# Kernel optimization log

Hardware: AMD Instinct MI355X
Metric: run time of the kernel (lower is better)

The kernel has to match this reference:

```python
import jax, jax.numpy as jnp
import numpy as np

ALPHA = 1.702  # sigmoid slope in clamped-GLU
LIMIT = 7.0    # clamp limit on gate/up

B, S, H, D, E, K = 2, 2048, 1024, 1024, 8, 2


def setup_inputs() -> dict:
    key = jax.random.key(0)
    ks = jax.random.split(key, 7)
    hidden_states = jax.random.normal(ks[0], (B, S, H), jnp.float32)
    router_indices = jax.random.randint(ks[1], (B * S, K), 0, E)
    routing_weights = jax.random.uniform(ks[2], (B * S, E), dtype=jnp.float32)
    gate_up_proj = jax.random.normal(ks[3], (E, H, 2 * D), jnp.float32) * 0.02
    gate_up_bias = jax.random.normal(ks[4], (E, 2 * D), jnp.float32) * 0.02
    down_proj = jax.random.normal(ks[5], (E, D, H), jnp.float32) * 0.02
    down_bias = jax.random.normal(ks[6], (E, H), jnp.float32) * 0.02
    return dict(hidden_states=hidden_states, router_indices=router_indices,
                routing_weights=routing_weights, gate_up_proj=gate_up_proj,
                gate_up_bias=gate_up_bias, down_proj=down_proj, down_bias=down_bias)


def reference(hidden_states, router_indices, routing_weights,
              gate_up_proj, gate_up_bias, down_proj, down_bias):
    batch = hidden_states.shape[0]
    hs = hidden_states.shape[-1]
    flat = hidden_states.reshape(-1, hs)  # [T, H]
    n_exp = routing_weights.shape[1]
    # index_add with possibly duplicated (token, expert) assignments == count multiplier
    counts = (router_indices[:, :, None] == jnp.arange(n_exp)[None, None, :]).sum(1)  # [T, E]
    w = routing_weights * counts.astype(flat.dtype)  # [T, E] effective combine weight

    def step(out, xs):
        wgu, bgu, wd, bd, we = xs  # wgu:[H,2D] bgu:[2D] wd:[D,H] bd:[H] we:[T]
        gu = flat @ wgu + bgu                      # [T, 2D]
        gate = jnp.minimum(gu[:, ::2], LIMIT)      # interleaved gate channels
        up = jnp.clip(gu[:, 1::2], -LIMIT, LIMIT)  # interleaved up channels
        mid = (up + 1.0) * gate * jax.nn.sigmoid(gate * ALPHA)
        y = mid @ wd + bd                          # [T, H]
        return out + y * we[:, None], None

    out0 = jnp.zeros_like(flat)
    out, _ = jax.lax.scan(step, out0, (gate_up_proj, gate_up_bias, down_proj, down_bias, w.T))
    return out.reshape(batch, -1, hs)
```

## Files before the change

### kernel.cpp

```cpp
#include <hip/hip_runtime.h>
#include <hip/hip_bf16.h>

#define AS1 __attribute__((address_space(1)))
#define AS3 __attribute__((address_space(3)))

typedef __bf16 bf16_8 __attribute__((ext_vector_type(8)));
typedef float f32x4 __attribute__((ext_vector_type(4)));

constexpr int Tn = 4096;
constexpr int Hn = 1024;
constexpr int Dn = 1024;
constexpr int En = 8;
constexpr int Pmax = 9216;
constexpr int MaxTiles = 72;
constexpr float kAlpha = 1.702f;
constexpr float kLimit = 7.0f;

__device__ __forceinline__ unsigned short f2bf(float x) {
  unsigned u = __builtin_bit_cast(unsigned, x);
  u = u + 0x7FFFu + ((u >> 16) & 1u);
  return (unsigned short)(u >> 16);
}
__device__ __forceinline__ unsigned pack2(float a, float b) {
  return (unsigned)f2bf(a) | ((unsigned)f2bf(b) << 16);
}
__device__ __forceinline__ float bflo(unsigned v) { return __builtin_bit_cast(float, v << 16); }
__device__ __forceinline__ float bfhi(unsigned v) { return __builtin_bit_cast(float, v & 0xFFFF0000u); }

__device__ __forceinline__ void gload_lds16(const void* gp, void* lp) {
  __builtin_amdgcn_global_load_lds(
      (const AS1 unsigned int*)(unsigned long long)gp,
      (AS3 unsigned int*)(unsigned int)(unsigned long long)lp,
      16, 0, 0);
}

constexpr int NB_CVT = 4096, NB_TGU = 4096, NB_TDN = 4096;
constexpr int NG1 = MaxTiles * (Dn / 64);

__global__ void k_prepass(const float* __restrict__ hs, const int* __restrict__ ridx,
                          const float* __restrict__ gup,
                          unsigned short* __restrict__ xb,
                          unsigned short* __restrict__ wg, unsigned short* __restrict__ wu,
                          int* __restrict__ tix, int* __restrict__ pos,
                          int* __restrict__ tileE, int* __restrict__ tileP0,
                          int* __restrict__ ntiles) {
  __shared__ __align__(16) char smem[2 * 32 * 65 * 4 + 64];
  const int tid = threadIdx.x;
  int b = blockIdx.x;

  if (b == 0) {
    int (*lh)[8] = (int(*)[8])smem;
    int* eoff = (int*)(smem + 8192);
#pragma unroll
    for (int e = 0; e < 8; e++) lh[tid][e] = 0;
    int myE[32];
#pragma unroll
    for (int s = 0; s < 32; s++) {
      int e = ridx[tid * 32 + s];
      myE[s] = e;
      lh[tid][e]++;
    }
    __syncthreads();
    if (tid < 8) {
      int tot = 0;
#pragma unroll 1
      for (int t = 0; t < 256; t++) { int v = lh[t][tid]; lh[t][tid] = tot; tot += v; }
      eoff[tid] = tot;
    }
    __syncthreads();
    if (tid == 0) {
      int off = 0, nt = 0;
#pragma unroll 1
      for (int e = 0; e < 8; e++) {
        int cnt = eoff[e];
        eoff[e] = off;
        int nt128 = (cnt + 127) >> 7;
        for (int k = 0; k < nt128; k++) { tileE[nt] = e; tileP0[nt] = off + k * 128; nt++; }
        off += nt128 * 128;
      }
      *ntiles = nt;
    }
    __syncthreads();
    for (int p = tid; p < Pmax; p += 256) tix[p] = 0;
    __syncthreads();
#pragma unroll
    for (int s = 0; s < 32; s++) {
      int slot = tid * 32 + s;
      int e = myE[s];
      int p = eoff[e] + (lh[tid][e]++);
      pos[slot] = p;
      tix[p] = slot >> 1;
    }
    return;
  }
  b -= 1;

  if (b < NB_CVT) {
    int i = b * 256 + tid;
    float4 v = reinterpret_cast<const float4*>(hs)[i];
    ushort4 o;
    o.x = f2bf(v.x); o.y = f2bf(v.y); o.z = f2bf(v.z); o.w = f2bf(v.w);
    reinterpret_cast<ushort4*>(xb)[i] = o;
    return;
  }
  b -= NB_CVT;

  {
    float (*lg)[65] = (float(*)[65])smem;
    float (*lu)[65] = (float(*)[65])(smem + 32 * 65 * 4);
    const int d0 = (b & 31) * 32, h0 = ((b >> 5) & 15) * 64, e = b >> 9;
    {
      const int hrow = tid >> 2, q = tid & 3;
      const float* src = gup + ((size_t)e * Hn + h0 + hrow) * (2 * Dn) + d0 * 2 + q * 16;
#pragma unroll
      for (int j = 0; j < 4; j++) {
        float4 v = *reinterpret_cast<const float4*>(src + j * 4);
        int dp = q * 8 + j * 2;
        lg[dp][hrow] = v.x; lu[dp][hrow] = v.y;
        lg[dp + 1][hrow] = v.z; lu[dp + 1][hrow] = v.w;
      }
    }
    __syncthreads();
    {
      const int d = tid >> 3, hc = (tid & 7) * 8;
      uint4 og, ou;
      og.x = pack2(lg[d][hc + 0], lg[d][hc + 1]); ou.x = pack2(lu[d][hc + 0], lu[d][hc + 1]);
      og.y = pack2(lg[d][hc + 2], lg[d][hc + 3]); ou.y = pack2(lu[d][hc + 2], lu[d][hc + 3]);
      og.z = pack2(lg[d][hc + 4], lg[d][hc + 5]); ou.z = pack2(lu[d][hc + 4], lu[d][hc + 5]);
      og.w = pack2(lg[d][hc + 6], lg[d][hc + 7]); ou.w = pack2(lu[d][hc + 6], lu[d][hc + 7]);
      *reinterpret_cast<uint4*>(wg + ((size_t)e * Dn + d0 + d) * Hn + h0 + hc) = og;
      *reinterpret_cast<uint4*>(wu + ((size_t)e * Dn + d0 + d) * Hn + h0 + hc) = ou;
    }
  }
}

__launch_bounds__(256, 2)
__global__ void k_main1(const unsigned short* __restrict__ xb,
                        const unsigned short* __restrict__ wg,
                        const unsigned short* __restrict__ wu,
                        const float* __restrict__ gub,
                        const int* __restrict__ tix,
                        const int* __restrict__ tileE,
                        const int* __restrict__ tileP0,
                        const int* __restrict__ ntiles,
                        unsigned short* __restrict__ midc,
                        const float* __restrict__ dwn,
                        unsigned short* __restrict__ wdt) {
  constexpr int BM = 128, BN = 64, BK = 64;
  __shared__ __align__(16) char smem[(BM + 2 * BN) * BK * 2];
  const int tid = threadIdx.x;

  if ((int)blockIdx.x >= NG1) {
    int b = blockIdx.x - NG1;
    float (*lt)[65] = (float(*)[65])smem;
    const int h0 = (b & 31) * 32, d0 = ((b >> 5) & 15) * 64, e = b >> 9;
    {
      const int drow = tid >> 2, q = tid & 3;
      const float* src = dwn + ((size_t)e * Dn + d0 + drow) * Hn + h0 + q * 8;
#pragma unroll
      for (int j = 0; j < 2; j++) {
        float4 v = *reinterpret_cast<const float4*>(src + j * 4);
        int hr = q * 8 + j * 4;
        lt[hr][drow] = v.x; lt[hr + 1][drow] = v.y; lt[hr + 2][drow] = v.z; lt[hr + 3][drow] = v.w;
      }
    }
    __syncthreads();
    {
      const int h = tid >> 3, dc = (tid & 7) * 8;
      uint4 o;
      o.x = pack2(lt[h][dc + 0], lt[h][dc + 1]);
      o.y = pack2(lt[h][dc + 2], lt[h][dc + 3]);
      o.z = pack2(lt[h][dc + 4], lt[h][dc + 5]);
      o.w = pack2(lt[h][dc + 6], lt[h][dc + 7]);
      *reinterpret_cast<uint4*>(wdt + ((size_t)e * Hn + h0 + h) * Dn + d0 + dc) = o;
    }
    return;
  }

  unsigned short* Xs = (unsigned short*)smem;
  unsigned short* Gs = (unsigned short*)(smem + BM * BK * 2);
  unsigned short* Us = (unsigned short*)(smem + (BM + BN) * BK * 2);
  const int orig = blockIdx.x;
  const int wgid = (orig & 7) * (NG1 >> 3) + (orig >> 3);
  const int bx = wgid % MaxTiles;
  const int by = wgid / MaxTiles;
  if (bx >= *ntiles) return;
  const int e = tileE[bx];
  const int p0 = tileP0[bx];
  const int n0 = by * BN;
  const int wv = tid >> 6, lane = tid & 63;
  const int wr = wv >> 1, wc = wv & 1;
  const int r8 = lane >> 3, c8 = lane & 7;

  int tokc[4];
#pragma unroll
  for (int c = 0; c < 4; c++) tokc[c] = tix[p0 + (c * 4 + wv) * 8 + r8];

  const unsigned short* Gp = wg + ((size_t)e * Dn + n0) * Hn;
  const unsigned short* Up = wu + ((size_t)e * Dn + n0) * Hn;

  f32x4 ag[4][2], au[4][2];
#pragma unroll
  for (int i = 0; i < 4; i++)
#pragma unroll
    for (int j = 0; j < 2; j++) { ag[i][j] = f32x4{0.f,0.f,0.f,0.f}; au[i][j] = f32x4{0.f,0.f,0.f,0.f}; }

  for (int k0 = 0; k0 < Hn; k0 += BK) {
#pragma unroll
    for (int c = 0; c < 4; c++) {
      int ch = c * 4 + wv;
      gload_lds16(xb + (size_t)tokc[c] * Hn + k0 + c8 * 8, (void*)(Xs + ch * 512));
    }
#pragma unroll
    for (int c = 0; c < 2; c++) {
      int ch = c * 4 + wv;
      gload_lds16(Gp + (size_t)(ch * 8 + r8) * Hn + k0 + c8 * 8, (void*)(Gs + ch * 512));
      gload_lds16(Up + (size_t)(ch * 8 + r8) * Hn + k0 + c8 * 8, (void*)(Us + ch * 512));
    }
    asm volatile("s_waitcnt vmcnt(0)" ::: "memory");
    __syncthreads();
    const int fr = lane & 15, kg = lane >> 4;
#pragma unroll
    for (int kk = 0; kk < 2; kk++) {
      bf16_8 a[4], bg[2], bu[2];
#pragma unroll
      for (int i = 0; i < 4; i++)
        a[i] = *reinterpret_cast<const bf16_8*>(Xs + (wr * 64 + i * 16 + fr) * BK + kk * 32 + kg * 8);
#pragma unroll
      for (int j = 0; j < 2; j++) {
        bg[j] = *reinterpret_cast<const bf16_8*>(Gs + (wc * 32 + j * 16 + fr) * BK + kk * 32 + kg * 8);
        bu[j] = *reinterpret_cast<const bf16_8*>(Us + (wc * 32 + j * 16 + fr) * BK + kk * 32 + kg * 8);
      }
#pragma unroll
      for (int i = 0; i < 4; i++)
#pragma unroll
        for (int j = 0; j < 2; j++) {
          ag[i][j] = __builtin_amdgcn_mfma_f32_16x16x32_bf16(a[i], bg[j], ag[i][j], 0, 0, 0);
          au[i][j] = __builtin_amdgcn_mfma_f32_16x16x32_bf16(a[i], bu[j], au[i][j], 0, 0, 0);
        }
    }
    __syncthreads();
  }

  const int fr = lane & 15, rg = lane >> 4;
  const float* gb = gub + e * 2 * Dn;
  const int dA = n0 + wc * 32 + fr, dB = dA + 16;
  const float gbiasA = gb[2 * dA], ubiasA = gb[2 * dA + 1];
  const float gbiasB = gb[2 * dB], ubiasB = gb[2 * dB + 1];
#pragma unroll
  for (int i = 0; i < 4; i++) {
#pragma unroll
    for (int r = 0; r < 4; r++) {
      int row = p0 + wr * 64 + i * 16 + rg * 4 + r;
#pragma unroll
      for (int j = 0; j < 2; j++) {
        int d = j ? dB : dA;
        float g = ag[i][j][r] + (j ? gbiasB : gbiasA);
        float u = au[i][j][r] + (j ? ubiasB : ubiasA);
        g = fminf(g, kLimit);
        u = fminf(fmaxf(u, -kLimit), kLimit);
        float sg = 1.0f / (1.0f + __expf(-kAlpha * g));
        float mid = (u + 1.0f) * g * sg;
        midc[(size_t)row * Dn + d] = f2bf(mid);
      }
    }
  }
}

__launch_bounds__(256, 2)
__global__ void k_gemm2(const unsigned short* __restrict__ midc,
                        const unsigned short* __restrict__ wdt,
                        const int* __restrict__ tileE,
                        const int* __restrict__ tileP0,
                        const int* __restrict__ ntiles,
                        unsigned short* __restrict__ ys) {
  constexpr int BM = 128, BN = 64, BK = 64;
  __shared__ __align__(16) unsigned short As[BM * BK];
  __shared__ __align__(16) unsigned short Bs[BN * BK];
  const int nwg = gridDim.x * gridDim.y;
  const int orig = blockIdx.y * gridDim.x + blockIdx.x;
  const int wgid = (orig & 7) * (nwg >> 3) + (orig >> 3);
  const int bx = wgid % gridDim.x;
  const int by = wgid / gridDim.x;
  if (bx >= *ntiles) return;
  const int e = tileE[bx];
  const int p0 = tileP0[bx];
  const int n0 = by * BN;
  const int tid = threadIdx.x;
  const int wv = tid >> 6, lane = tid & 63;
  const int wr = wv >> 1, wc = wv & 1;
  const int r8 = lane >> 3, c8 = lane & 7;
  const unsigned short* Ap = midc + (size_t)p0 * Dn;
  const unsigned short* Bp = wdt + ((size_t)e * Hn + n0) * Dn;

  f32x4 acc[4][2];
#pragma unroll
  for (int i = 0; i < 4; i++)
#pragma unroll
    for (int j = 0; j < 2; j++) acc[i][j] = f32x4{0.f,0.f,0.f,0.f};

  for (int k0 = 0; k0 < Dn; k0 += BK) {
#pragma unroll
    for (int c = 0; c < 4; c++) {
      int ch = c * 4 + wv;
      gload_lds16(Ap + (size_t)(ch * 8 + r8) * Dn + k0 + c8 * 8, (void*)(As + ch * 512));
    }
#pragma unroll
    for (int c = 0; c < 2; c++) {
      int ch = c * 4 + wv;
      gload_lds16(Bp + (size_t)(ch * 8 + r8) * Dn + k0 + c8 * 8, (void*)(Bs + ch * 512));
    }
    asm volatile("s_waitcnt vmcnt(0)" ::: "memory");
    __syncthreads();
    const int fr = lane & 15, kg = lane >> 4;
#pragma unroll
    for (int kk = 0; kk < 2; kk++) {
      bf16_8 a[4], b[2];
#pragma unroll
      for (int i = 0; i < 4; i++)
        a[i] = *reinterpret_cast<const bf16_8*>(As + (wr * 64 + i * 16 + fr) * BK + kk * 32 + kg * 8);
#pragma unroll
      for (int j = 0; j < 2; j++)
        b[j] = *reinterpret_cast<const bf16_8*>(Bs + (wc * 32 + j * 16 + fr) * BK + kk * 32 + kg * 8);
#pragma unroll
      for (int i = 0; i < 4; i++)
#pragma unroll
        for (int j = 0; j < 2; j++)
          acc[i][j] = __builtin_amdgcn_mfma_f32_16x16x32_bf16(a[i], b[j], acc[i][j], 0, 0, 0);
    }
    __syncthreads();
  }

  const int fr = lane & 15, rg = lane >> 4;
#pragma unroll
  for (int i = 0; i < 4; i++)
#pragma unroll
    for (int r = 0; r < 4; r++) {
      int row = p0 + wr * 64 + i * 16 + rg * 4 + r;
#pragma unroll
      for (int j = 0; j < 2; j++) {
        int col = n0 + wc * 32 + j * 16 + fr;
        ys[(size_t)row * Hn + col] = f2bf(acc[i][j][r]);
      }
    }
}

__global__ void k_combine(const unsigned short* __restrict__ ys, const int* __restrict__ ridx,
                          const float* __restrict__ rw, const int* __restrict__ pos,
                          const float* __restrict__ db, float* __restrict__ out) {
  int idx = blockIdx.x * blockDim.x + threadIdx.x;
  int t = idx >> 7, hc = (idx & 127) << 3;
  int e0 = ridx[2 * t], e1 = ridx[2 * t + 1];
  int p0 = pos[2 * t], p1 = pos[2 * t + 1];
  float w0 = rw[t * En + e0], w1 = rw[t * En + e1];
  uint4 ya = *reinterpret_cast<const uint4*>(ys + (size_t)p0 * Hn + hc);
  uint4 yb = *reinterpret_cast<const uint4*>(ys + (size_t)p1 * Hn + hc);
  float4 da0 = *reinterpret_cast<const float4*>(db + (size_t)e0 * Hn + hc);
  float4 da1 = *reinterpret_cast<const float4*>(db + (size_t)e0 * Hn + hc + 4);
  float4 db0 = *reinterpret_cast<const float4*>(db + (size_t)e1 * Hn + hc);
  float4 db1 = *reinterpret_cast<const float4*>(db + (size_t)e1 * Hn + hc + 4);
  float4 o0, o1;
  o0.x = w0 * (bflo(ya.x) + da0.x) + w1 * (bflo(yb.x) + db0.x);
  o0.y = w0 * (bfhi(ya.x) + da0.y) + w1 * (bfhi(yb.x) + db0.y);
  o0.z = w0 * (bflo(ya.y) + da0.z) + w1 * (bflo(yb.y) + db0.z);
  o0.w = w0 * (bfhi(ya.y) + da0.w) + w1 * (bfhi(yb.y) + db0.w);
  o1.x = w0 * (bflo(ya.z) + da1.x) + w1 * (bflo(yb.z) + db1.x);
  o1.y = w0 * (bfhi(ya.z) + da1.y) + w1 * (bfhi(yb.z) + db1.y);
  o1.z = w0 * (bflo(ya.w) + da1.z) + w1 * (bflo(yb.w) + db1.z);
  o1.w = w0 * (bfhi(ya.w) + da1.w) + w1 * (bfhi(yb.w) + db1.w);
  *reinterpret_cast<float4*>(out + (size_t)t * Hn + hc) = o0;
  *reinterpret_cast<float4*>(out + (size_t)t * Hn + hc + 4) = o1;
}

extern "C" void kernel_launch(void* const* d_in, const int* in_sizes, int n_in,
                              void* d_out, int out_size, void* d_ws, size_t ws_size,
                              hipStream_t stream) {
  (void)in_sizes; (void)n_in; (void)out_size; (void)ws_size;
  const float* hs  = (const float*)d_in[0];
  const int*   ri  = (const int*)d_in[1];
  const float* rw  = (const float*)d_in[2];
  const float* gup = (const float*)d_in[3];
  const float* gub = (const float*)d_in[4];
  const float* dwn = (const float*)d_in[5];
  const float* db  = (const float*)d_in[6];
  float* out = (float*)d_out;

  char* ws = (char*)d_ws;
  int* tix    = (int*)(ws);
  int* pos    = (int*)(ws + 65536);
  int* tileE  = (int*)(ws + 131072);
  int* tileP0 = (int*)(ws + 131584);
  int* ntiles = (int*)(ws + 132096);
  unsigned short* xb   = (unsigned short*)(ws + 262144);
  unsigned short* wg   = (unsigned short*)(ws + 262144 + 8388608);
  unsigned short* wu   = (unsigned short*)(ws + 262144 + 8388608 + 16777216);
  unsigned short* wdt  = (unsigned short*)(ws + 262144 + 8388608 + 2*16777216);
  unsigned short* midc = (unsigned short*)(ws + 262144 + 8388608 + 3*16777216);
  unsigned short* ys   = (unsigned short*)(ws + 262144 + 8388608 + 3*16777216 + (size_t)Pmax * Dn * 2);

  k_prepass<<<dim3(1 + NB_CVT + NB_TGU), dim3(256), 0, stream>>>(
      hs, ri, gup, xb, wg, wu, tix, pos, tileE, tileP0, ntiles);
  k_main1<<<dim3(NG1 + NB_TDN), dim3(256), 0, stream>>>(
      xb, wg, wu, gub, tix, tileE, tileP0, ntiles, midc, dwn, wdt);
  k_gemm2<<<dim3(MaxTiles, Hn / 64), dim3(256), 0, stream>>>(
      midc, wdt, tileE, tileP0, ntiles, ys);
  k_combine<<<dim3(Tn * Hn / 8 / 256), dim3(256), 0, stream>>>(ys, ri, rw, pos, db, out);
}
```

Measured before the change: 138.7 us.

## Enlarge expert row tiles to 256 and give each wave a full-width output strip

Per-expert token groups are now padded to 256 rows instead of 128. Both grouped GEMMs use 256-row tiles with flattened 1D grids. Each wave now owns 64 rows across the whole tile width and issues a 4x4 MFMA block per k-step, replacing the previous 2x2 wave grid. In the first GEMM the gate and up weight slices share one 64-column LDS buffer over 32 output channels. The aim is more reuse per LDS fragment load and fewer redundant activation gathers, at the cost of more padding rows, fewer blocks in the second GEMM and higher register pressure, with launch bounds raised to 3 blocks per CU.

```diff
diff --git a/kernel.cpp b/kernel.cpp
--- a/kernel.cpp
+++ b/kernel.cpp
@@ -11,8 +11,8 @@
 constexpr int Hn = 1024;
 constexpr int Dn = 1024;
 constexpr int En = 8;
-constexpr int Pmax = 9216;
-constexpr int MaxTiles = 72;
+constexpr int Pmax = 10240;
+constexpr int MaxT256 = 40;
 constexpr float kAlpha = 1.702f;
 constexpr float kLimit = 7.0f;
 
@@ -35,7 +35,7 @@
 }
 
 constexpr int NB_CVT = 4096, NB_TGU = 4096, NB_TDN = 4096;
-constexpr int NG1 = MaxTiles * (Dn / 64);
+constexpr int NG1 = MaxT256 * 32;
 
 __global__ void k_prepass(const float* __restrict__ hs, const int* __restrict__ ridx,
                           const float* __restrict__ gup,
@@ -74,9 +74,9 @@
       for (int e = 0; e < 8; e++) {
         int cnt = eoff[e];
         eoff[e] = off;
-        int nt128 = (cnt + 127) >> 7;
-        for (int k = 0; k < nt128; k++) { tileE[nt] = e; tileP0[nt] = off + k * 128; nt++; }
-        off += nt128 * 128;
+        int ntT = (cnt + 255) >> 8;
+        for (int k = 0; k < ntT; k++) { tileE[nt] = e; tileP0[nt] = off + k * 256; nt++; }
+        off += ntT * 256;
       }
       *ntiles = nt;
     }
@@ -134,7 +134,7 @@
   }
 }
 
-__launch_bounds__(256, 2)
+__launch_bounds__(256, 3)
 __global__ void k_main1(const unsigned short* __restrict__ xb,
                         const unsigned short* __restrict__ wg,
                         const unsigned short* __restrict__ wu,
@@ -146,8 +146,7 @@
                         unsigned short* __restrict__ midc,
                         const float* __restrict__ dwn,
                         unsigned short* __restrict__ wdt) {
-  constexpr int BM = 128, BN = 64, BK = 64;
-  __shared__ __align__(16) char smem[(BM + 2 * BN) * BK * 2];
+  __shared__ __align__(16) char smem[40960];
   const int tid = threadIdx.x;
 
   if ((int)blockIdx.x >= NG1) {
@@ -178,130 +177,126 @@
   }
 
   unsigned short* Xs = (unsigned short*)smem;
-  unsigned short* Gs = (unsigned short*)(smem + BM * BK * 2);
-  unsigned short* Us = (unsigned short*)(smem + (BM + BN) * BK * 2);
+  unsigned short* Bs = (unsigned short*)(smem + 32768);
   const int orig = blockIdx.x;
   const int wgid = (orig & 7) * (NG1 >> 3) + (orig >> 3);
-  const int bx = wgid % MaxTiles;
-  const int by = wgid / MaxTiles;
+  const int by = wgid & 31;
+  const int bx = wgid >> 5;
   if (bx >= *ntiles) return;
   const int e = tileE[bx];
   const int p0 = tileP0[bx];
-  const int n0 = by * BN;
+  const int n0 = by * 32;
   const int wv = tid >> 6, lane = tid & 63;
-  const int wr = wv >> 1, wc = wv & 1;
   const int r8 = lane >> 3, c8 = lane & 7;
-
-  int tokc[4];
-#pragma unroll
-  for (int c = 0; c < 4; c++) tokc[c] = tix[p0 + (c * 4 + wv) * 8 + r8];
+  const int fr = lane & 15, kg = lane >> 4;
+
+  int tokc[8];
+#pragma unroll
+  for (int c = 0; c < 8; c++) tokc[c] = tix[p0 + (c * 4 + wv) * 8 + r8];
 
   const unsigned short* Gp = wg + ((size_t)e * Dn + n0) * Hn;
   const unsigned short* Up = wu + ((size_t)e * Dn + n0) * Hn;
 
-  f32x4 ag[4][2], au[4][2];
+  f32x4 acc[4][4];
 #pragma unroll
   for (int i = 0; i < 4; i++)
 #pragma unroll
-    for (int j = 0; j < 2; j++) { ag[i][j] = f32x4{0.f,0.f,0.f,0.f}; au[i][j] = f32x4{0.f,0.f,0.f,0.f}; }
-
-  for (int k0 = 0; k0 < Hn; k0 += BK) {
-#pragma unroll
-    for (int c = 0; c < 4; c++) {
+    for (int j = 0; j < 4; j++) acc[i][j] = f32x4{0.f, 0.f, 0.f, 0.f};
+
+  for (int k0 = 0; k0 < Hn; k0 += 64) {
+#pragma unroll
+    for (int c = 0; c < 8; c++) {
       int ch = c * 4 + wv;
       gload_lds16(xb + (size_t)tokc[c] * Hn + k0 + c8 * 8, (void*)(Xs + ch * 512));
     }
-#pragma unroll
-    for (int c = 0; c < 2; c++) {
-      int ch = c * 4 + wv;
-      gload_lds16(Gp + (size_t)(ch * 8 + r8) * Hn + k0 + c8 * 8, (void*)(Gs + ch * 512));
-      gload_lds16(Up + (size_t)(ch * 8 + r8) * Hn + k0 + c8 * 8, (void*)(Us + ch * 512));
+    {
+      gload_lds16(Gp + (size_t)(wv * 8 + r8) * Hn + k0 + c8 * 8, (void*)(Bs + wv * 512));
+      gload_lds16(Up + (size_t)(wv * 8 + r8) * Hn + k0 + c8 * 8, (void*)(Bs + (wv + 4) * 512));
     }
     asm volatile("s_waitcnt vmcnt(0)" ::: "memory");
     __syncthreads();
-    const int fr = lane & 15, kg = lane >> 4;
 #pragma unroll
     for (int kk = 0; kk < 2; kk++) {
-      bf16_8 a[4], bg[2], bu[2];
+      bf16_8 a[4], b[4];
 #pragma unroll
       for (int i = 0; i < 4; i++)
-        a[i] = *reinterpret_cast<const bf16_8*>(Xs + (wr * 64 + i * 16 + fr) * BK + kk * 32 + kg * 8);
-#pragma unroll
-      for (int j = 0; j < 2; j++) {
-        bg[j] = *reinterpret_cast<const bf16_8*>(Gs + (wc * 32 + j * 16 + fr) * BK + kk * 32 + kg * 8);
-        bu[j] = *reinterpret_cast<const bf16_8*>(Us + (wc * 32 + j * 16 + fr) * BK + kk * 32 + kg * 8);
-      }
+        a[i] = *reinterpret_cast<const bf16_8*>(Xs + (wv * 64 + i * 16 + fr) * 64 + kk * 32 + kg * 8);
+#pragma unroll
+      for (int j = 0; j < 4; j++)
+        b[j] = *reinterpret_cast<const bf16_8*>(Bs + (j * 16 + fr) * 64 + kk * 32 + kg * 8);
 #pragma unroll
       for (int i = 0; i < 4; i++)
 #pragma unroll
-        for (int j = 0; j < 2; j++) {
-          ag[i][j] = __builtin_amdgcn_mfma_f32_16x16x32_bf16(a[i], bg[j], ag[i][j], 0, 0, 0);
-          au[i][j] = __builtin_amdgcn_mfma_f32_16x16x32_bf16(a[i], bu[j], au[i][j], 0, 0, 0);
-        }
-    }
-    __syncthreads();
-  }
-
-  const int fr = lane & 15, rg = lane >> 4;
+        for (int j = 0; j < 4; j++)
+          acc[i][j] = __builtin_amdgcn_mfma_f32_16x16x32_bf16(a[i], b[j], acc[i][j], 0, 0, 0);
+    }
+    __syncthreads();
+  }
+
+  const int rg = kg;
   const float* gb = gub + e * 2 * Dn;
-  const int dA = n0 + wc * 32 + fr, dB = dA + 16;
-  const float gbiasA = gb[2 * dA], ubiasA = gb[2 * dA + 1];
-  const float gbiasB = gb[2 * dB], ubiasB = gb[2 * dB + 1];
+  const int d0 = n0 + fr, d1 = n0 + 16 + fr;
+  const float gb0 = gb[2 * d0], ub0 = gb[2 * d0 + 1];
+  const float gb1 = gb[2 * d1], ub1 = gb[2 * d1 + 1];
 #pragma unroll
   for (int i = 0; i < 4; i++) {
 #pragma unroll
     for (int r = 0; r < 4; r++) {
-      int row = p0 + wr * 64 + i * 16 + rg * 4 + r;
-#pragma unroll
-      for (int j = 0; j < 2; j++) {
-        int d = j ? dB : dA;
-        float g = ag[i][j][r] + (j ? gbiasB : gbiasA);
-        float u = au[i][j][r] + (j ? ubiasB : ubiasA);
+      int row = p0 + wv * 64 + i * 16 + rg * 4 + r;
+      {
+        float g = acc[i][0][r] + gb0;
+        float u = acc[i][2][r] + ub0;
         g = fminf(g, kLimit);
         u = fminf(fmaxf(u, -kLimit), kLimit);
         float sg = 1.0f / (1.0f + __expf(-kAlpha * g));
-        float mid = (u + 1.0f) * g * sg;
-        midc[(size_t)row * Dn + d] = f2bf(mid);
-      }
-    }
-  }
-}
-
-__launch_bounds__(256, 2)
+        midc[(size_t)row * Dn + d0] = f2bf((u + 1.0f) * g * sg);
+      }
+      {
+        float g = acc[i][1][r] + gb1;
+        float u = acc[i][3][r] + ub1;
+        g = fminf(g, kLimit);
+        u = fminf(fmaxf(u, -kLimit), kLimit);
+        float sg = 1.0f / (1.0f + __expf(-kAlpha * g));
+        midc[(size_t)row * Dn + d1] = f2bf((u + 1.0f) * g * sg);
+      }
+    }
+  }
+}
+
+__launch_bounds__(256, 3)
 __global__ void k_gemm2(const unsigned short* __restrict__ midc,
                         const unsigned short* __restrict__ wdt,
                         const int* __restrict__ tileE,
                         const int* __restrict__ tileP0,
                         const int* __restrict__ ntiles,
                         unsigned short* __restrict__ ys) {
-  constexpr int BM = 128, BN = 64, BK = 64;
-  __shared__ __align__(16) unsigned short As[BM * BK];
-  __shared__ __align__(16) unsigned short Bs[BN * BK];
-  const int nwg = gridDim.x * gridDim.y;
-  const int orig = blockIdx.y * gridDim.x + blockIdx.x;
+  __shared__ __align__(16) unsigned short As[256 * 64];
+  __shared__ __align__(16) unsigned short Bs[64 * 64];
+  const int nwg = gridDim.x;
+  const int orig = blockIdx.x;
   const int wgid = (orig & 7) * (nwg >> 3) + (orig >> 3);
-  const int bx = wgid % gridDim.x;
-  const int by = wgid / gridDim.x;
+  const int by = wgid & 15;
+  const int bx = wgid >> 4;
   if (bx >= *ntiles) return;
   const int e = tileE[bx];
   const int p0 = tileP0[bx];
-  const int n0 = by * BN;
+  const int n0 = by * 64;
   const int tid = threadIdx.x;
   const int wv = tid >> 6, lane = tid & 63;
-  const int wr = wv >> 1, wc = wv & 1;
   const int r8 = lane >> 3, c8 = lane & 7;
+  const int fr = lane & 15, kg = lane >> 4;
   const unsigned short* Ap = midc + (size_t)p0 * Dn;
   const unsigned short* Bp = wdt + ((size_t)e * Hn + n0) * Dn;
 
-  f32x4 acc[4][2];
+  f32x4 acc[4][4];
 #pragma unroll
   for (int i = 0; i < 4; i++)
 #pragma unroll
-    for (int j = 0; j < 2; j++) acc[i][j] = f32x4{0.f,0.f,0.f,0.f};
-
-  for (int k0 = 0; k0 < Dn; k0 += BK) {
-#pragma unroll
-    for (int c = 0; c < 4; c++) {
+    for (int j = 0; j < 4; j++) acc[i][j] = f32x4{0.f, 0.f, 0.f, 0.f};
+
+  for (int k0 = 0; k0 < Dn; k0 += 64) {
+#pragma unroll
+    for (int c = 0; c < 8; c++) {
       int ch = c * 4 + wv;
       gload_lds16(Ap + (size_t)(ch * 8 + r8) * Dn + k0 + c8 * 8, (void*)(As + ch * 512));
     }
@@ -312,34 +307,33 @@
     }
     asm volatile("s_waitcnt vmcnt(0)" ::: "memory");
     __syncthreads();
-    const int fr = lane & 15, kg = lane >> 4;
 #pragma unroll
     for (int kk = 0; kk < 2; kk++) {
-      bf16_8 a[4], b[2];
+      bf16_8 a[4], b[4];
 #pragma unroll
       for (int i = 0; i < 4; i++)
-        a[i] = *reinterpret_cast<const bf16_8*>(As + (wr * 64 + i * 16 + fr) * BK + kk * 32 + kg * 8);
-#pragma unroll
-      for (int j = 0; j < 2; j++)
-        b[j] = *reinterpret_cast<const bf16_8*>(Bs + (wc * 32 + j * 16 + fr) * BK + kk * 32 + kg * 8);
+        a[i] = *reinterpret_cast<const bf16_8*>(As + (wv * 64 + i * 16 + fr) * 64 + kk * 32 + kg * 8);
+#pragma unroll
+      for (int j = 0; j < 4; j++)
+        b[j] = *reinterpret_cast<const bf16_8*>(Bs + (j * 16 + fr) * 64 + kk * 32 + kg * 8);
 #pragma unroll
       for (int i = 0; i < 4; i++)
 #pragma unroll
-        for (int j = 0; j < 2; j++)
+        for (int j = 0; j < 4; j++)
           acc[i][j] = __builtin_amdgcn_mfma_f32_16x16x32_bf16(a[i], b[j], acc[i][j], 0, 0, 0);
     }
     __syncthreads();
   }
 
-  const int fr = lane & 15, rg = lane >> 4;
+  const int rg = kg;
 #pragma unroll
   for (int i = 0; i < 4; i++)
 #pragma unroll
     for (int r = 0; r < 4; r++) {
-      int row = p0 + wr * 64 + i * 16 + rg * 4 + r;
-#pragma unroll
-      for (int j = 0; j < 2; j++) {
-        int col = n0 + wc * 32 + j * 16 + fr;
+      int row = p0 + wv * 64 + i * 16 + rg * 4 + r;
+#pragma unroll
+      for (int j = 0; j < 4; j++) {
+        int col = n0 + j * 16 + fr;
         ys[(size_t)row * Hn + col] = f2bf(acc[i][j][r]);
       }
     }
@@ -402,7 +396,7 @@
       hs, ri, gup, xb, wg, wu, tix, pos, tileE, tileP0, ntiles);
   k_main1<<<dim3(NG1 + NB_TDN), dim3(256), 0, stream>>>(
       xb, wg, wu, gub, tix, tileE, tileP0, ntiles, midc, dwn, wdt);
-  k_gemm2<<<dim3(MaxTiles, Hn / 64), dim3(256), 0, stream>>>(
+  k_gemm2<<<dim3(MaxT256 * 16), dim3(256), 0, stream>>>(
       midc, wdt, tileE, tileP0, ntiles, ys);
   k_combine<<<dim3(Tn * Hn / 8 / 256), dim3(256), 0, stream>>>(ys, ri, rw, pos, db, out);
 }
```

After: 131.1 us. 5.5% less time.
